# Performance work log

Hardware: AMD Instinct MI355X
Metric: run time of the kernel (lower is better)

Reference implementation:

```python
import jax, jax.numpy as jnp
import numpy as np

N_NODES = 5000
N_EDGES = 40000
NUM_ATOM_TYPES = 100
HID = 32            # multiplicity of 0e and 1o in irreps_hidden
EDGE_ATTR_DIM = 8
NUM_BOND_TYPES = 5
OUT_SCALARS = 2 * 6 + 1  # max_charge=6 -> 13x0e
CUTOFF = 5.0
SQRT3 = 1.7320508075688772


def _sh(edge_vec):
    # o3.SphericalHarmonics('1x0e + 1x1o', normalize=True, normalization='component')
    d = jnp.sqrt(jnp.sum(edge_vec * edge_vec, axis=-1) + 1e-12)
    n = edge_vec / d[:, None]
    sh0 = jnp.ones(edge_vec.shape[0], edge_vec.dtype)          # [E]
    sh1 = SQRT3 * n[:, (1, 2, 0)]                              # [E,3], e3nn (y,z,x) order
    return sh0, sh1, d


def _soft_one_hot(d):
    # e3nn.math.soft_one_hot_linspace(d, 0, cutoff, 8, basis='gaussian', cutoff=True)
    values = jnp.linspace(0.0, CUTOFF, EDGE_ATTR_DIM + 2)[1:-1]
    step = CUTOFF / (EDGE_ATTR_DIM + 1)
    diff = (d[:, None] - values[None, :]) / step
    return jnp.exp(-diff * diff) / 1.12


def _mlp(x, W0, b0, W1, b1):
    # ScalarMLP(in, out, hidden=[in], SiLU)
    return jax.nn.silu(x @ W0 + b0) @ W1 + b1


def _tp_init(s, sh0, sh1, w):
    # FCTP(32x0e, 1x0e+1x1o -> 32x0e+32x1o); paths: 0e*0e->0e, 0e*1o->1o
    E = s.shape[0]
    w1 = w[:, : HID * HID].reshape(E, HID, HID)
    w2 = w[:, HID * HID :].reshape(E, HID, HID)
    c = 1.0 / np.sqrt(HID)  # fan-in = 32 per output irrep
    out_s = c * jnp.einsum('eu,euw->ew', s * sh0[:, None], w1)
    out_v = c * jnp.einsum('eu,ei,euw->ewi', s, sh1, w2)
    return out_s, out_v


def _tp_hidden(s, v, sh0, sh1, w):
    # FCTP(32x0e+32x1o, 1x0e+1x1o -> 32x0e+32x1o)
    # path order: 0e*0e->0e, 0e*1o->1o, 1o*0e->1o, 1o*1o->0e
    E = s.shape[0]
    ws = w.reshape(E, 4, HID, HID)
    c = 1.0 / np.sqrt(2 * HID)  # fan-in = 64 per output irrep
    dot = jnp.einsum('eui,ei->eu', v, sh1) / SQRT3  # CG(1,1->0) = delta/sqrt(3)
    out_s = c * (jnp.einsum('eu,euw->ew', s * sh0[:, None], ws[:, 0]) +
                 jnp.einsum('eu,euw->ew', dot, ws[:, 3]))
    out_v = c * (jnp.einsum('eu,ei,euw->ewi', s, sh1, ws[:, 1]) +
                 jnp.einsum('eui,euw->ewi', v * sh0[:, None, None], ws[:, 2]))
    return out_s, out_v


def _edge_tp(s1, v1, s2, v2, sh0, sh1, w):
    # FCTP(64x0e+64x1o (concat of two hidden), 1x0e+1x1o -> 5x0e)
    # blocks in concat order: s_src, v_src, s_dst, v_dst
    E = s1.shape[0]
    ws = w.reshape(E, 4, HID, NUM_BOND_TYPES)
    c = 1.0 / np.sqrt(4 * HID)  # fan-in = 128
    d1 = jnp.einsum('eui,ei->eu', v1, sh1) / SQRT3
    d2 = jnp.einsum('eui,ei->eu', v2, sh1) / SQRT3
    return c * (jnp.einsum('eu,euw->ew', s1 * sh0[:, None], ws[:, 0]) +
                jnp.einsum('eu,euw->ew', d1, ws[:, 1]) +
                jnp.einsum('eu,euw->ew', s2 * sh0[:, None], ws[:, 2]) +
                jnp.einsum('eu,euw->ew', d2, ws[:, 3]))


def _scatter_mean(ms, mv, dst, n):
    cnt = jax.ops.segment_sum(jnp.ones(dst.shape[0], ms.dtype), dst, num_segments=n)
    cnt = jnp.maximum(cnt, 1.0)
    s = jax.ops.segment_sum(ms, dst, num_segments=n) / cnt[:, None]
    v = jax.ops.segment_sum(mv, dst, num_segments=n) / cnt[:, None, None]
    return s, v


def setup_inputs() -> dict:
    key = jax.random.key(0)
    ks = jax.random.split(key, 16)
    def w(k, shape, fan_in):
        return jax.random.normal(k, shape, dtype=jnp.float32) / np.sqrt(fan_in)
    inp = {}
    inp['coordinates'] = jax.random.normal(ks[0], (N_NODES, 3), dtype=jnp.float32) * 1.5
    inp['atom_types'] = jax.random.randint(ks[1], (N_NODES,), 0, NUM_ATOM_TYPES)
    inp['edge_index'] = jax.random.randint(ks[2], (2, N_EDGES), 0, N_NODES)
    inp['atom_embed'] = jax.random.normal(ks[3], (NUM_ATOM_TYPES, HID), dtype=jnp.float32)
    inp['ip_W0'] = w(ks[4], (EDGE_ATTR_DIM, EDGE_ATTR_DIM), EDGE_ATTR_DIM)
    inp['ip_b0'] = jnp.zeros((EDGE_ATTR_DIM,), jnp.float32)
    inp['ip_W1'] = w(ks[5], (EDGE_ATTR_DIM, 2 * HID * HID), EDGE_ATTR_DIM)
    inp['ip_b1'] = jnp.zeros((2 * HID * HID,), jnp.float32)
    inp['ly_W0'] = w(ks[6], (EDGE_ATTR_DIM, EDGE_ATTR_DIM), EDGE_ATTR_DIM)
    inp['ly_b0'] = jnp.zeros((EDGE_ATTR_DIM,), jnp.float32)
    inp['ly_W1'] = w(ks[7], (EDGE_ATTR_DIM, 4 * HID * HID), EDGE_ATTR_DIM)
    inp['ly_b1'] = jnp.zeros((4 * HID * HID,), jnp.float32)
    inp['ly_Ws'] = jax.random.normal(ks[8], (HID, HID), dtype=jnp.float32)
    inp['ly_Wv'] = jax.random.normal(ks[9], (HID, HID), dtype=jnp.float32)
    inp['et_W0'] = w(ks[10], (EDGE_ATTR_DIM, EDGE_ATTR_DIM), EDGE_ATTR_DIM)
    inp['et_b0'] = jnp.zeros((EDGE_ATTR_DIM,), jnp.float32)
    inp['et_W1'] = w(ks[11], (EDGE_ATTR_DIM, 4 * HID * NUM_BOND_TYPES), EDGE_ATTR_DIM)
    inp['et_b1'] = jnp.zeros((4 * HID * NUM_BOND_TYPES,), jnp.float32)
    inp['no_W1'] = jax.random.normal(ks[12], (HID, OUT_SCALARS), dtype=jnp.float32)
    inp['no_W2'] = jax.random.normal(ks[13], (OUT_SCALARS, OUT_SCALARS), dtype=jnp.float32)
    return inp


def reference(coordinates, atom_types, edge_index, atom_embed,
              ip_W0, ip_b0, ip_W1, ip_b1,
              ly_W0, ly_b0, ly_W1, ly_b1, ly_Ws, ly_Wv,
              et_W0, et_b0, et_W1, et_b1, no_W1, no_W2):
    n = coordinates.shape[0]
    src, dst = edge_index[0], edge_index[1]
    edge_vec = coordinates[dst] - coordinates[src]
    sh0, sh1, d = _sh(edge_vec)
    edge_attr = _soft_one_hot(d)                              # [E,8]
    # initial projector: Conv(32x0e -> 32x0e+32x1o)
    s0 = atom_embed[atom_types]                               # [N,32]
    w_ip = _mlp(edge_attr, ip_W0, ip_b0, ip_W1, ip_b1)        # [E,2048]
    ms, mv = _tp_init(s0[src], sh0, sh1, w_ip)
    s, v = _scatter_mean(ms, mv, dst, n)                      # [N,32],[N,32,3]
    # one LinearSelfInteraction(Conv) layer
    w_ly = _mlp(edge_attr, ly_W0, ly_b0, ly_W1, ly_b1)        # [E,4096]
    ms, mv = _tp_hidden(s[src], v[src], sh0, sh1, w_ly)
    cs, cv = _scatter_mean(ms, mv, dst, n)
    lc = 1.0 / np.sqrt(HID)  # e3nn o3.Linear normalization
    s = cs + lc * (s @ ly_Ws)
    v = cv + lc * jnp.einsum('eui,uw->ewi', v, ly_Wv)
    # edge output: FCTP([h_src, h_dst], edge_sh) with radial weights
    w_et = _mlp(edge_attr, et_W0, et_b0, et_W1, et_b1)        # [E,640]
    edge_out = _edge_tp(s[src], v[src], s[dst], v[dst], sh0, sh1, w_et)  # [E,5]
    # node output MLP on detached scalar channel (13x0e)
    sd = jax.lax.stop_gradient(s)
    h = jax.nn.silu(sd @ no_W1 / np.sqrt(HID))
    node_out = h @ no_W2 / np.sqrt(OUT_SCALARS)               # [N,13]
    return edge_out, node_out
```

## Files before the change

### kernel.cpp

```cpp
#include <hip/hip_runtime.h>

#define NN 5000
#define NE 40000
#define HB 625

typedef unsigned int u32;
typedef unsigned short u16;
typedef __fp16 h16x2 __attribute__((ext_vector_type(2)));
typedef _Float16 f16x8 __attribute__((ext_vector_type(8)));
typedef __attribute__((ext_vector_type(4))) float f32x4;

union AF { u32 u[4]; f16x8 v; uint4 q; };

__device__ __forceinline__ float siluf(float x) { return x / (1.f + __expf(-x)); }

__device__ __forceinline__ u32 f2bf_u(float f) {
  u32 x = __float_as_uint(f);
  return (x + 0x7FFFu + ((x >> 16) & 1u)) >> 16;
}
__device__ __forceinline__ u16 f2bf(float f) { return (u16)f2bf_u(f); }
__device__ __forceinline__ float bf2f(u16 v) { return __uint_as_float(((u32)v) << 16); }
__device__ __forceinline__ u32 packbf2(float lo, float hi) {
  return f2bf_u(lo) | (f2bf_u(hi) << 16);
}
__device__ __forceinline__ u32 pkh2(float a, float b) {
  union { h16x2 h; u32 u; } r;
  r.h = __builtin_amdgcn_cvt_pkrtz(a, b);
  return r.u;
}
__device__ __forceinline__ u16 f2h(float v) {
  _Float16 h = (_Float16)v;
  return *(u16*)&h;
}
__device__ __forceinline__ void unpack8(uint4 q, float* f) {
  f[0] = __uint_as_float(q.x << 16); f[1] = __uint_as_float(q.x & 0xFFFF0000u);
  f[2] = __uint_as_float(q.y << 16); f[3] = __uint_as_float(q.y & 0xFFFF0000u);
  f[4] = __uint_as_float(q.z << 16); f[5] = __uint_as_float(q.z & 0xFFFF0000u);
  f[6] = __uint_as_float(q.w << 16); f[7] = __uint_as_float(q.w & 0xFFFF0000u);
}
__device__ __forceinline__ float dot8f(const float* h, const float* w, float init) {
  float a = init;
#pragma unroll
  for (int k = 0; k < 8; k++) a = fmaf(h[k], w[k], a);
  return a;
}
__device__ __forceinline__ void mlp8(const float* ea, const float* __restrict__ W0,
                                     const float* __restrict__ b0, float* h) {
#pragma unroll
  for (int j = 0; j < 8; j++) {
    float a = b0[j];
#pragma unroll
    for (int i = 0; i < 8; i++) a += ea[i] * W0[i*8 + j];
    h[j] = siluf(a);
  }
}
__device__ __forceinline__ AF mkfrag(float hs, const float* s) {
  AF a;
  a.u[0] = pkh2(hs*s[0], hs*s[1]);
  a.u[1] = pkh2(hs*s[2], hs*s[3]);
  a.u[2] = pkh2(hs*s[4], hs*s[5]);
  a.u[3] = pkh2(hs*s[6], hs*s[7]);
  return a;
}

__global__ __launch_bounds__(256) void k_conv1g(
    const float* __restrict__ coords, const int* __restrict__ eidx,
    const float* __restrict__ emb, const int* __restrict__ atype,
    const float* __restrict__ ipW0, const float* __restrict__ ipb0,
    const float* __restrict__ lyW0, const float* __restrict__ lyb0,
    const float* __restrict__ etW0, const float* __restrict__ etb0,
    const float* __restrict__ W1, const float* __restrict__ b1,
    const float* __restrict__ lyW1, const float* __restrict__ lyb1,
    float* __restrict__ sh, float* __restrict__ h_ly, float* __restrict__ h_et,
    int* __restrict__ cur, int* __restrict__ perm,
    u16* __restrict__ msg, u16* __restrict__ lyT) {
  if (blockIdx.x >= HB) {
    int b = blockIdx.x - HB;
    int h = b >> 3;
    int t0 = (b & 7)*2304 + threadIdx.x*9;
#pragma unroll
    for (int j = 0; j < 9; j++) {
      int t = t0 + j;
      int kch = t >> 9, rem = t & 511;
      int col = rem >> 3, kk = rem & 7;
      int k = kch*8 + kk;
      int basec = (h == 0) ? ((col >> 5)*1024 + (col & 31))
                           : ((col < 32) ? (2048 + col) : (3072 + (col - 32)));
      float v = (k < 256) ? lyW1[(k >> 5)*4096 + basec + (k & 31)*32]
                          : lyb1[basec + (k - 256)*32];
      lyT[h*18432 + t] = f2h(v);
    }
    return;
  }
  __shared__ __align__(16) u16 B2[36*64*8];
  __shared__ float hl[64][9];
  __shared__ float shl[64][4];
  __shared__ int   sAl[64];
  {
    int col = threadIdx.x & 63, pth = col >> 5, w = col & 31;
    int k0 = (threadIdx.x >> 6) * 72;
    for (int k = k0; k < k0 + 72; k++) {
      float v = (k < 256) ? W1[(k >> 5)*2048 + pth*1024 + (k & 31)*32 + w]
                          : b1[pth*1024 + (k - 256)*32 + w];
      B2[((k >> 3)*64 + col)*8 + (k & 7)] = f2h(v);
    }
  }
  if (threadIdx.x < 64) {
    int idx = threadIdx.x;
    int w = (idx >> 4) & 3, m = idx & 15;
    int tile = blockIdx.x*4 + w;
    int e = tile*16 + m;
    int s = eidx[e], d = eidx[NE + e];
    float vx = coords[d*3+0] - coords[s*3+0];
    float vy = coords[d*3+1] - coords[s*3+1];
    float vz = coords[d*3+2] - coords[s*3+2];
    float dist = sqrtf(vx*vx + vy*vy + vz*vz + 1e-12f);
    float inv = 1.f / dist;
    const float SQ3 = 1.7320508075688772f;
    float s0 = SQ3 * vy * inv;
    float s1 = SQ3 * vz * inv;
    float s2 = SQ3 * vx * inv;
    sh[e*3+0] = s0; sh[e*3+1] = s1; sh[e*3+2] = s2;
    shl[idx][0] = s0; shl[idx][1] = s1; shl[idx][2] = s2;
    sAl[idx] = atype[s];
    float ea[8];
    const float step = 5.f / 9.f;
#pragma unroll
    for (int jj = 0; jj < 8; jj++) {
      float diff = (dist - step * (float)(jj+1)) * (9.f / 5.f);
      ea[jj] = __expf(-diff*diff) * (1.f / 1.12f);
    }
    float h[8];
    mlp8(ea, ipW0, ipb0, h);
#pragma unroll
    for (int jj = 0; jj < 8; jj++) hl[idx][jj] = h[jj];
    mlp8(ea, lyW0, lyb0, h);
    { float4 f0 = {h[0],h[1],h[2],h[3]}, f1 = {h[4],h[5],h[6],h[7]};
      *(float4*)&h_ly[e*8] = f0; *(float4*)&h_ly[e*8+4] = f1; }
    mlp8(ea, etW0, etb0, h);
    { float4 f0 = {h[0],h[1],h[2],h[3]}, f1 = {h[4],h[5],h[6],h[7]};
      *(float4*)&h_et[e*8] = f0; *(float4*)&h_et[e*8+4] = f1; }
    int* cp = &cur[d];
    atomicCAS(cp, (int)0xAAAAAAAA, 0);
    int t = atomicAdd(cp, 1);
    if (t < 64) perm[d*64 + t] = e;
  }
  __syncthreads();
  int lane = threadIdx.x & 63;
  int m = lane & 15, q = lane >> 4, wid = threadIdx.x >> 6;
  const float cs = 0.17677669529663687f;
  int tile = blockIdx.x*4 + wid;
  {
    int le = wid*16 + m;
    int srow = sAl[le];
    float4 sA = *(const float4*)&emb[srow*32 + q*8];
    float4 sB = *(const float4*)&emb[srow*32 + q*8 + 4];
    float sf[8] = {sA.x,sA.y,sA.z,sA.w,sB.x,sB.y,sB.z,sB.w};
    float hf[8];
#pragma unroll
    for (int k = 0; k < 8; k++) hf[k] = hl[le][k];
    f32x4 acc0 = {0.f,0.f,0.f,0.f}, acc1 = acc0, acc2 = acc0, acc3 = acc0;
#pragma unroll
    for (int ks = 0; ks < 9; ks++) {
      float hs = (ks < 8) ? hf[ks] : 1.f;
      AF a = mkfrag(hs, sf);
      int c2 = (ks*4 + q)*64;
      AF b0, b1f, b2, b3;
      b0.q  = *(const uint4*)&B2[(c2 +  0 + m)*8];
      b1f.q = *(const uint4*)&B2[(c2 + 16 + m)*8];
      b2.q  = *(const uint4*)&B2[(c2 + 32 + m)*8];
      b3.q  = *(const uint4*)&B2[(c2 + 48 + m)*8];
      acc0 = __builtin_amdgcn_mfma_f32_16x16x32_f16(a.v, b0.v,  acc0, 0, 0, 0);
      acc1 = __builtin_amdgcn_mfma_f32_16x16x32_f16(a.v, b1f.v, acc1, 0, 0, 0);
      acc2 = __builtin_amdgcn_mfma_f32_16x16x32_f16(a.v, b2.v,  acc2, 0, 0, 0);
      acc3 = __builtin_amdgcn_mfma_f32_16x16x32_f16(a.v, b3.v,  acc3, 0, 0, 0);
    }
#pragma unroll
    for (int r = 0; r < 4; r++) {
      int lr = wid*16 + q*4 + r;
      int et = tile*16 + q*4 + r;
      u16* mp = msg + (size_t)et*128;
      mp[m]      = f2bf(cs*acc0[r]);
      mp[16 + m] = f2bf(cs*acc1[r]);
      float s0v = shl[lr][0], s1v = shl[lr][1], s2v = shl[lr][2];
      float m0 = cs*acc2[r], m1 = cs*acc3[r];
      mp[32 +      m] = f2bf(m0*s0v);
      mp[64 +      m] = f2bf(m0*s1v);
      mp[96 +      m] = f2bf(m0*s2v);
      mp[32 + 16 + m] = f2bf(m1*s0v);
      mp[64 + 16 + m] = f2bf(m1*s1v);
      mp[96 + 16 + m] = f2bf(m1*s2v);
    }
  }
}

__global__ __launch_bounds__(256) void k_conv2(
    const float* __restrict__ hE, const float* __restrict__ sh,
    const float* __restrict__ s1, const float* __restrict__ v1soa,
    const int* __restrict__ eidx, const u16* __restrict__ lyT,
    u16* __restrict__ msgA, u16* __restrict__ msgB) {
  __shared__ __align__(16) u16 B2[36*64*8];
  const bool scalarHalf = blockIdx.x < HB;
  int blk = scalarHalf ? blockIdx.x : blockIdx.x - HB;
  {
    const uint4* src4 = (const uint4*)(lyT + (scalarHalf ? 0 : 18432));
    uint4* dst4 = (uint4*)B2;
    for (int t = threadIdx.x; t < 2304; t += 256) dst4[t] = src4[t];
  }
  __syncthreads();
  int lane = threadIdx.x & 63;
  int m = lane & 15, q = lane >> 4, wid = threadIdx.x >> 6;
  const float c = 0.125f;
  int tile = blk*4 + wid;
  {
    int e = tile*16 + m;
    int srcn = eidx[e];
    float4 hA = *(const float4*)&hE[e*8];
    float4 hB = *(const float4*)&hE[e*8 + 4];
    float hf[8] = {hA.x,hA.y,hA.z,hA.w,hB.x,hB.y,hB.z,hB.w};

    if (scalarHalf) {
      float4 sA = *(const float4*)&s1[srcn*32 + q*8];
      float4 sB = *(const float4*)&s1[srcn*32 + q*8 + 4];
      float sf[8] = {sA.x,sA.y,sA.z,sA.w,sB.x,sB.y,sB.z,sB.w};
      f32x4 acc0 = {0.f,0.f,0.f,0.f}, acc1 = acc0, acc2 = acc0, acc3 = acc0;
#pragma unroll
      for (int ks = 0; ks < 9; ks++) {
        float hs = (ks < 8) ? hf[ks] : 1.f;
        AF a = mkfrag(hs, sf);
        int c2 = (ks*4 + q)*64;
        AF b0, b1f, b2, b3;
        b0.q  = *(const uint4*)&B2[(c2 +  0 + m)*8];
        b1f.q = *(const uint4*)&B2[(c2 + 16 + m)*8];
        b2.q  = *(const uint4*)&B2[(c2 + 32 + m)*8];
        b3.q  = *(const uint4*)&B2[(c2 + 48 + m)*8];
        acc0 = __builtin_amdgcn_mfma_f32_16x16x32_f16(a.v, b0.v,  acc0, 0, 0, 0);
        acc1 = __builtin_amdgcn_mfma_f32_16x16x32_f16(a.v, b1f.v, acc1, 0, 0, 0);
        acc2 = __builtin_amdgcn_mfma_f32_16x16x32_f16(a.v, b2.v,  acc2, 0, 0, 0);
        acc3 = __builtin_amdgcn_mfma_f32_16x16x32_f16(a.v, b3.v,  acc3, 0, 0, 0);
      }
#pragma unroll
      for (int r = 0; r < 4; r++) {
        int et = tile*16 + q*4 + r;
        u16* mp = msgA + (size_t)et*128;
        mp[m]      = f2bf(c*acc0[r]);
        mp[16 + m] = f2bf(c*acc1[r]);
        float s0v = sh[et*3+0], s1v = sh[et*3+1], s2v = sh[et*3+2];
        float m0 = c*acc2[r], m1 = c*acc3[r];
        mp[32 +      m] = f2bf(m0*s0v);
        mp[64 +      m] = f2bf(m0*s1v);
        mp[96 +      m] = f2bf(m0*s2v);
        mp[32 + 16 + m] = f2bf(m1*s0v);
        mp[64 + 16 + m] = f2bf(m1*s1v);
        mp[96 + 16 + m] = f2bf(m1*s2v);
      }
    } else {
      const float is3 = 0.5773502691896258f;
      float vf[3][8];
#pragma unroll
      for (int i = 0; i < 3; i++) {
        float4 aa = *(const float4*)&v1soa[i*160000 + srcn*32 + q*8];
        float4 bb = *(const float4*)&v1soa[i*160000 + srcn*32 + q*8 + 4];
        vf[i][0]=aa.x; vf[i][1]=aa.y; vf[i][2]=aa.z; vf[i][3]=aa.w;
        vf[i][4]=bb.x; vf[i][5]=bb.y; vf[i][6]=bb.z; vf[i][7]=bb.w;
      }
      float es0 = sh[e*3+0], es1 = sh[e*3+1], es2 = sh[e*3+2];
      float df[8];
#pragma unroll
      for (int j = 0; j < 8; j++)
        df[j] = (vf[0][j]*es0 + vf[1][j]*es1 + vf[2][j]*es2) * is3;
      f32x4 z = {0.f,0.f,0.f,0.f};
      f32x4 aV00 = z, aV01 = z, aV10 = z, aV11 = z, aV20 = z, aV21 = z, aD0 = z, aD1 = z;
#pragma unroll
      for (int ks = 0; ks < 9; ks++) {
        float hs = (ks < 8) ? hf[ks] : 1.f;
        int c2 = (ks*4 + q)*64;
        AF b0, b1f, b2, b3;
        b0.q  = *(const uint4*)&B2[(c2 +  0 + m)*8];
        b1f.q = *(const uint4*)&B2[(c2 + 16 + m)*8];
        b2.q  = *(const uint4*)&B2[(c2 + 32 + m)*8];
        b3.q  = *(const uint4*)&B2[(c2 + 48 + m)*8];
        AF a0 = mkfrag(hs, vf[0]);
        AF a1 = mkfrag(hs, vf[1]);
        AF a2 = mkfrag(hs, vf[2]);
        AF ad = mkfrag(hs, df);
        aV00 = __builtin_amdgcn_mfma_f32_16x16x32_f16(a0.v, b0.v,  aV00, 0, 0, 0);
        aV01 = __builtin_amdgcn_mfma_f32_16x16x32_f16(a0.v, b1f.v, aV01, 0, 0, 0);
        aV10 = __builtin_amdgcn_mfma_f32_16x16x32_f16(a1.v, b0.v,  aV10, 0, 0, 0);
        aV11 = __builtin_amdgcn_mfma_f32_16x16x32_f16(a1.v, b1f.v, aV11, 0, 0, 0);
        aV20 = __builtin_amdgcn_mfma_f32_16x16x32_f16(a2.v, b0.v,  aV20, 0, 0, 0);
        aV21 = __builtin_amdgcn_mfma_f32_16x16x32_f16(a2.v, b1f.v, aV21, 0, 0, 0);
        aD0  = __builtin_amdgcn_mfma_f32_16x16x32_f16(ad.v, b2.v,  aD0,  0, 0, 0);
        aD1  = __builtin_amdgcn_mfma_f32_16x16x32_f16(ad.v, b3.v,  aD1,  0, 0, 0);
      }
#pragma unroll
      for (int r = 0; r < 4; r++) {
        int et = tile*16 + q*4 + r;
        u16* mp = msgB + (size_t)et*128;
        mp[m]      = f2bf(c*aD0[r]);
        mp[16 + m] = f2bf(c*aD1[r]);
        mp[32 +      m] = f2bf(c*aV00[r]);
        mp[32 + 16 + m] = f2bf(c*aV01[r]);
        mp[64 +      m] = f2bf(c*aV10[r]);
        mp[64 + 16 + m] = f2bf(c*aV11[r]);
        mp[96 +      m] = f2bf(c*aV20[r]);
        mp[96 + 16 + m] = f2bf(c*aV21[r]);
      }
    }
  }
}

__global__ __launch_bounds__(256) void k_gather1(
    const u16* __restrict__ msg, const int* __restrict__ perm,
    const int* __restrict__ cur, float* __restrict__ s1,
    float* __restrict__ v1soa) {
  __shared__ int pe[2][64];
  int ln = threadIdx.x >> 7, c = threadIdx.x & 127;
  int n = blockIdx.x*2 + ln;
  int deg = min(cur[n], 64);
  if (c < 64) pe[ln][c] = perm[n*64 + c];
  __syncthreads();
  float acc = 0.f;
  int j = 0;
  for (; j + 4 <= deg; j += 4) {
    int e0 = pe[ln][j], e1 = pe[ln][j+1], e2 = pe[ln][j+2], e3 = pe[ln][j+3];
    float x0 = bf2f(msg[(size_t)e0*128 + c]);
    float x1 = bf2f(msg[(size_t)e1*128 + c]);
    float x2 = bf2f(msg[(size_t)e2*128 + c]);
    float x3 = bf2f(msg[(size_t)e3*128 + c]);
    acc += (x0 + x1) + (x2 + x3);
  }
  for (; j < deg; j++)
    acc += bf2f(msg[(size_t)pe[ln][j]*128 + c]);
  acc /= (float)max(deg, 1);
  if (c < 32) s1[n*32 + c] = acc;
  else { int i = (c-32) >> 5, w = (c-32) & 31; v1soa[i*160000 + n*32 + w] = acc; }
}

__global__ __launch_bounds__(256) void k_gather2(
    const u16* __restrict__ msgA, const u16* __restrict__ msgB,
    const int* __restrict__ perm, const int* __restrict__ cur,
    const float* __restrict__ s1, const float* __restrict__ v1soa,
    const float* __restrict__ Ws, const float* __restrict__ Wv,
    const float* __restrict__ noW1, const float* __restrict__ noW2,
    float* __restrict__ s2, float* __restrict__ v2, float* __restrict__ outN) {
  __shared__ int pe[2][64];
  __shared__ float sb[2][32];
  __shared__ float hb[2][13];
  int ln = threadIdx.x >> 7, c = threadIdx.x & 127;
  int n = blockIdx.x*2 + ln;
  int deg = min(cur[n], 64);
  if (c < 64) pe[ln][c] = perm[n*64 + c];
  __syncthreads();
  float acc = 0.f;
  int j = 0;
  for (; j + 4 <= deg; j += 4) {
    int e0 = pe[ln][j], e1 = pe[ln][j+1], e2 = pe[ln][j+2], e3 = pe[ln][j+3];
    float x0 = bf2f(msgA[(size_t)e0*128 + c]) + bf2f(msgB[(size_t)e0*128 + c]);
    float x1 = bf2f(msgA[(size_t)e1*128 + c]) + bf2f(msgB[(size_t)e1*128 + c]);
    float x2 = bf2f(msgA[(size_t)e2*128 + c]) + bf2f(msgB[(size_t)e2*128 + c]);
    float x3 = bf2f(msgA[(size_t)e3*128 + c]) + bf2f(msgB[(size_t)e3*128 + c]);
    acc += (x0 + x1) + (x2 + x3);
  }
  for (; j < deg; j++) {
    int e = pe[ln][j];
    acc += bf2f(msgA[(size_t)e*128 + c]) + bf2f(msgB[(size_t)e*128 + c]);
  }
  acc /= (float)max(deg, 1);
  const float lc = 0.17677669529663687f;
  if (c < 32) {
    float ss = 0.f;
#pragma unroll 8
    for (int u = 0; u < 32; u++) ss += s1[n*32 + u] * Ws[u*32 + c];
    float val = acc + lc*ss;
    s2[n*32 + c] = val;
    sb[ln][c] = val;
  } else {
    int i = (c-32) >> 5, w = (c-32) & 31;
    float sv = 0.f;
#pragma unroll 8
    for (int u = 0; u < 32; u++) sv += v1soa[i*160000 + n*32 + u] * Wv[u*32 + w];
    v2[n*96 + w*3 + i] = acc + lc*sv;
  }
  __syncthreads();
  const float i32 = 0.17677669529663687f;
  if (c < 13) {
    float a = 0.f;
#pragma unroll 8
    for (int u = 0; u < 32; u++) a += sb[ln][u] * noW1[u*13 + c];
    hb[ln][c] = siluf(a * i32);
  }
  __syncthreads();
  const float i13 = 0.2773500981126146f;
  if (c < 13) {
    float a = 0.f;
#pragma unroll
    for (int j2 = 0; j2 < 13; j2++) a += hb[ln][j2] * noW2[j2*13 + c];
    outN[n*13 + c] = a * i13;
  }
}

__global__ __launch_bounds__(256) void k_e3(
    const float* __restrict__ hE, const float* __restrict__ sh,
    const float* __restrict__ s2, const float* __restrict__ v2,
    const int* __restrict__ eidx,
    const float* __restrict__ W1, const float* __restrict__ b1,
    float* __restrict__ out) {
  __shared__ uint4 WQ[640];
  __shared__ float BQ[640];
  for (int t = threadIdx.x; t < 640; t += 256) {
    int u = t & 31, pw = t >> 5, p2 = pw / 5, w = pw - p2*5;
    int col = p2*160 + u*5 + w;
    const float* s = W1 + col;
    uint4 q;
    q.x = packbf2(s[0],      s[640]);
    q.y = packbf2(s[1280],   s[1920]);
    q.z = packbf2(s[2560],   s[3200]);
    q.w = packbf2(s[3840],   s[4480]);
    WQ[t] = q;
    BQ[t] = b1[col];
  }
  __syncthreads();
  const int g = threadIdx.x >> 5, tw = threadIdx.x & 31;
  const float c = 0.08838834764831845f;
  const float is3 = 0.5773502691896258f;
  for (int p = blockIdx.x*8 + g; p*2 < NE; p += gridDim.x*8) {
    int e0 = p*2, e1 = e0 + 1;
    float h0[8], h1[8];
    {
      float4 qa = *(const float4*)&hE[e0*8];
      float4 qb = *(const float4*)&hE[e0*8+4];
      h0[0]=qa.x; h0[1]=qa.y; h0[2]=qa.z; h0[3]=qa.w;
      h0[4]=qb.x; h0[5]=qb.y; h0[6]=qb.z; h0[7]=qb.w;
      float4 qc = *(const float4*)&hE[e1*8];
      float4 qd = *(const float4*)&hE[e1*8+4];
      h1[0]=qc.x; h1[1]=qc.y; h1[2]=qc.z; h1[3]=qc.w;
      h1[4]=qd.x; h1[5]=qd.y; h1[6]=qd.z; h1[7]=qd.w;
    }
    int sA = eidx[e0], dA = eidx[NE+e0];
    int sB = eidx[e1], dB = eidx[NE+e1];
    float sa0 = sh[e0*3+0], sa1 = sh[e0*3+1], sa2 = sh[e0*3+2];
    float sb0 = sh[e1*3+0], sb1 = sh[e1*3+1], sb2 = sh[e1*3+2];
    float c00 = s2[sA*32 + tw];
    float c01 = (v2[sA*96+tw*3+0]*sa0 + v2[sA*96+tw*3+1]*sa1 + v2[sA*96+tw*3+2]*sa2) * is3;
    float c02 = s2[dA*32 + tw];
    float c03 = (v2[dA*96+tw*3+0]*sa0 + v2[dA*96+tw*3+1]*sa1 + v2[dA*96+tw*3+2]*sa2) * is3;
    float c10 = s2[sB*32 + tw];
    float c11 = (v2[sB*96+tw*3+0]*sb0 + v2[sB*96+tw*3+1]*sb1 + v2[sB*96+tw*3+2]*sb2) * is3;
    float c12 = s2[dB*32 + tw];
    float c13 = (v2[dB*96+tw*3+0]*sb0 + v2[dB*96+tw*3+1]*sb1 + v2[dB*96+tw*3+2]*sb2) * is3;
    float part0[5] = {0,0,0,0,0};
    float part1[5] = {0,0,0,0,0};
#pragma unroll
    for (int pp = 0; pp < 4; pp++) {
      float cp0 = (pp==0) ? c00 : (pp==1) ? c01 : (pp==2) ? c02 : c03;
      float cp1 = (pp==0) ? c10 : (pp==1) ? c11 : (pp==2) ? c12 : c13;
#pragma unroll
      for (int w = 0; w < 5; w++) {
        int idx = (pp*5 + w)*32 + tw;
        float f[8];
        unpack8(WQ[idx], f);
        float bv = BQ[idx];
        part0[w] = fmaf(cp0, dot8f(h0, f, bv), part0[w]);
        part1[w] = fmaf(cp1, dot8f(h1, f, bv), part1[w]);
      }
    }
#pragma unroll
    for (int off = 16; off > 0; off >>= 1)
#pragma unroll
      for (int w = 0; w < 5; w++) {
        part0[w] += __shfl_xor(part0[w], off, 32);
        part1[w] += __shfl_xor(part1[w], off, 32);
      }
    float outv = 0.f;
#pragma unroll
    for (int w = 0; w < 5; w++) {
      if (tw == w)     outv = part0[w];
      if (tw == 5 + w) outv = part1[w];
    }
    if (tw < 10) out[e0*5 + tw] = c * outv;
  }
}

extern "C" void kernel_launch(void* const* d_in, const int* in_sizes, int n_in,
                              void* d_out, int out_size, void* d_ws, size_t ws_size,
                              hipStream_t stream) {
  (void)in_sizes; (void)n_in; (void)out_size; (void)ws_size;
  const float* coords = (const float*)d_in[0];
  const int*   atype  = (const int*)d_in[1];
  const int*   eidx   = (const int*)d_in[2];
  const float* emb    = (const float*)d_in[3];
  const float* ipW0 = (const float*)d_in[4];
  const float* ipb0 = (const float*)d_in[5];
  const float* ipW1 = (const float*)d_in[6];
  const float* ipb1 = (const float*)d_in[7];
  const float* lyW0 = (const float*)d_in[8];
  const float* lyb0 = (const float*)d_in[9];
  const float* lyW1 = (const float*)d_in[10];
  const float* lyb1 = (const float*)d_in[11];
  const float* lyWs = (const float*)d_in[12];
  const float* lyWv = (const float*)d_in[13];
  const float* etW0 = (const float*)d_in[14];
  const float* etb0 = (const float*)d_in[15];
  const float* etW1 = (const float*)d_in[16];
  const float* etb1 = (const float*)d_in[17];
  const float* noW1 = (const float*)d_in[18];
  const float* noW2 = (const float*)d_in[19];

  float* ws = (float*)d_ws;
  float* sh    = ws;
  float* h_ly  = ws + 440000;
  float* h_et  = ws + 760000;
  float* s1    = ws + 1240000;
  float* v1soa = ws + 1400000;
  float* s2    = ws + 1880000;
  float* v2    = ws + 2040000;
  int*   cur   = (int*)(ws + 2520000);
  int*   perm  = (int*)(ws + 2525000);
  u16*   msgA  = (u16*)(ws + 2845000);
  u16*   msgB  = (u16*)(ws + 5405000);
  u16*   lyT   = (u16*)(ws + 7965000);

  float* outE = (float*)d_out;
  float* outN = (float*)d_out + NE*5;

  k_conv1g<<<HB + 16, 256, 0, stream>>>(coords, eidx, emb, atype,
                                        ipW0, ipb0, lyW0, lyb0, etW0, etb0,
                                        ipW1, ipb1, lyW1, lyb1,
                                        sh, h_ly, h_et, cur, perm, msgA, lyT);
  k_gather1<<<NN/2, 256, 0, stream>>>(msgA, perm, cur, s1, v1soa);
  k_conv2<<<2*HB, 256, 0, stream>>>(h_ly, sh, s1, v1soa, eidx, lyT, msgA, msgB);
  k_gather2<<<NN/2, 256, 0, stream>>>(msgA, msgB, perm, cur, s1, v1soa,
                                      lyWs, lyWv, noW1, noW2, s2, v2, outN);
  k_e3<<<2500, 256, 0, stream>>>(h_et, sh, s2, v2, eidx, etW1, etb1, outE);
}
```

Before: 177.9 us.

## Read transposed weights from global memory instead of staging in LDS, add prep kernel

Adds a separate prep kernel that converts the initial-projector and layer weights to fp16 MFMA layout, so the conv kernels read B fragments directly from global/L2 instead of filling shared memory per block. k_conv1 now has every lane compute edge geometry and the radial MLP redundantly, and uses shuffles instead of LDS and barriers. The k_e3 grid drops from 2500 to 1024 blocks. It trades LDS fill and sync cost for redundant ALU work, repeated global weight reads and one extra launch.

Result: faster. 164.9 us (-7.3%).

```diff
diff --git a/kernel.cpp b/kernel.cpp
--- a/kernel.cpp
+++ b/kernel.cpp
@@ -2,7 +2,6 @@
 
 #define NN 5000
 #define NE 40000
-#define HB 625
 
 typedef unsigned int u32;
 typedef unsigned short u16;
@@ -19,7 +18,6 @@
   return (x + 0x7FFFu + ((x >> 16) & 1u)) >> 16;
 }
 __device__ __forceinline__ u16 f2bf(float f) { return (u16)f2bf_u(f); }
-__device__ __forceinline__ float bf2f(u16 v) { return __uint_as_float(((u32)v) << 16); }
 __device__ __forceinline__ u32 packbf2(float lo, float hi) {
   return f2bf_u(lo) | (f2bf_u(hi) << 16);
 }
@@ -63,19 +61,12 @@
   return a;
 }
 
-__global__ __launch_bounds__(256) void k_conv1g(
-    const float* __restrict__ coords, const int* __restrict__ eidx,
-    const float* __restrict__ emb, const int* __restrict__ atype,
-    const float* __restrict__ ipW0, const float* __restrict__ ipb0,
-    const float* __restrict__ lyW0, const float* __restrict__ lyb0,
-    const float* __restrict__ etW0, const float* __restrict__ etb0,
-    const float* __restrict__ W1, const float* __restrict__ b1,
+__global__ __launch_bounds__(256) void k_prep(
+    const float* __restrict__ ipW1, const float* __restrict__ ipb1,
     const float* __restrict__ lyW1, const float* __restrict__ lyb1,
-    float* __restrict__ sh, float* __restrict__ h_ly, float* __restrict__ h_et,
-    int* __restrict__ cur, int* __restrict__ perm,
-    u16* __restrict__ msg, u16* __restrict__ lyT) {
-  if (blockIdx.x >= HB) {
-    int b = blockIdx.x - HB;
+    u16* __restrict__ ipT, u16* __restrict__ lyT) {
+  int b = blockIdx.x;
+  if (b < 16) {
     int h = b >> 3;
     int t0 = (b & 7)*2304 + threadIdx.x*9;
 #pragma unroll
@@ -90,75 +81,129 @@
                           : lyb1[basec + (k - 256)*32];
       lyT[h*18432 + t] = f2h(v);
     }
-    return;
-  }
-  __shared__ __align__(16) u16 B2[36*64*8];
-  __shared__ float hl[64][9];
-  __shared__ float shl[64][4];
-  __shared__ int   sAl[64];
-  {
-    int col = threadIdx.x & 63, pth = col >> 5, w = col & 31;
-    int k0 = (threadIdx.x >> 6) * 72;
-    for (int k = k0; k < k0 + 72; k++) {
-      float v = (k < 256) ? W1[(k >> 5)*2048 + pth*1024 + (k & 31)*32 + w]
-                          : b1[pth*1024 + (k - 256)*32 + w];
-      B2[((k >> 3)*64 + col)*8 + (k & 7)] = f2h(v);
-    }
-  }
-  if (threadIdx.x < 64) {
-    int idx = threadIdx.x;
-    int w = (idx >> 4) & 3, m = idx & 15;
-    int tile = blockIdx.x*4 + w;
-    int e = tile*16 + m;
-    int s = eidx[e], d = eidx[NE + e];
-    float vx = coords[d*3+0] - coords[s*3+0];
-    float vy = coords[d*3+1] - coords[s*3+1];
-    float vz = coords[d*3+2] - coords[s*3+2];
-    float dist = sqrtf(vx*vx + vy*vy + vz*vz + 1e-12f);
-    float inv = 1.f / dist;
-    const float SQ3 = 1.7320508075688772f;
-    float s0 = SQ3 * vy * inv;
-    float s1 = SQ3 * vz * inv;
-    float s2 = SQ3 * vx * inv;
-    sh[e*3+0] = s0; sh[e*3+1] = s1; sh[e*3+2] = s2;
-    shl[idx][0] = s0; shl[idx][1] = s1; shl[idx][2] = s2;
-    sAl[idx] = atype[s];
-    float ea[8];
-    const float step = 5.f / 9.f;
-#pragma unroll
-    for (int jj = 0; jj < 8; jj++) {
-      float diff = (dist - step * (float)(jj+1)) * (9.f / 5.f);
-      ea[jj] = __expf(-diff*diff) * (1.f / 1.12f);
-    }
-    float h[8];
-    mlp8(ea, ipW0, ipb0, h);
-#pragma unroll
-    for (int jj = 0; jj < 8; jj++) hl[idx][jj] = h[jj];
-    mlp8(ea, lyW0, lyb0, h);
-    { float4 f0 = {h[0],h[1],h[2],h[3]}, f1 = {h[4],h[5],h[6],h[7]};
+  } else {
+    int t0 = (b - 16)*2304 + threadIdx.x*9;
+#pragma unroll
+    for (int j = 0; j < 9; j++) {
+      int t = t0 + j;
+      int kch = t >> 9, rem = t & 511;
+      int col = rem >> 3, kk = rem & 7;
+      int k = kch*8 + kk;
+      int pth = col >> 5, w = col & 31;
+      float v = (k < 256) ? ipW1[(k >> 5)*2048 + pth*1024 + (k & 31)*32 + w]
+                          : ipb1[pth*1024 + (k - 256)*32 + w];
+      ipT[t] = f2h(v);
+    }
+  }
+}
+
+__global__ __launch_bounds__(256) void k_conv1(
+    const float* __restrict__ coords, const int* __restrict__ eidx,
+    const float* __restrict__ emb, const int* __restrict__ atype,
+    const float* __restrict__ ipW0, const float* __restrict__ ipb0,
+    const float* __restrict__ lyW0, const float* __restrict__ lyb0,
+    const float* __restrict__ etW0, const float* __restrict__ etb0,
+    const u16* __restrict__ ipT,
+    float* __restrict__ sh, float* __restrict__ h_ly, float* __restrict__ h_et,
+    int* __restrict__ cur, int* __restrict__ perm, u16* __restrict__ msg) {
+  int wid = threadIdx.x >> 6, lane = threadIdx.x & 63;
+  int tile = blockIdx.x*4 + wid;
+  int m = lane & 15, q = lane >> 4;
+  int e = tile*16 + m;
+  int s = eidx[e], d = eidx[NE + e];
+  float vx = coords[d*3+0] - coords[s*3+0];
+  float vy = coords[d*3+1] - coords[s*3+1];
+  float vz = coords[d*3+2] - coords[s*3+2];
+  float dist = sqrtf(vx*vx + vy*vy + vz*vz + 1e-12f);
+  float dinv = 1.f / dist;
+  const float SQ3 = 1.7320508075688772f;
+  float sh0 = SQ3 * vy * dinv;
+  float sh1 = SQ3 * vz * dinv;
+  float sh2 = SQ3 * vx * dinv;
+  int srow = atype[s];
+  float ea[8];
+  const float step = 5.f / 9.f;
+#pragma unroll
+  for (int jj = 0; jj < 8; jj++) {
+    float diff = (dist - step * (float)(jj+1)) * (9.f / 5.f);
+    ea[jj] = __expf(-diff*diff) * (1.f / 1.12f);
+  }
+  float hip[8], hly[8], het[8];
+  mlp8(ea, ipW0, ipb0, hip);
+  mlp8(ea, lyW0, lyb0, hly);
+  mlp8(ea, etW0, etb0, het);
+  if (q == 0) {
+    sh[e*3+0] = sh0; sh[e*3+1] = sh1; sh[e*3+2] = sh2;
+    { float4 f0 = {hly[0],hly[1],hly[2],hly[3]}, f1 = {hly[4],hly[5],hly[6],hly[7]};
       *(float4*)&h_ly[e*8] = f0; *(float4*)&h_ly[e*8+4] = f1; }
-    mlp8(ea, etW0, etb0, h);
-    { float4 f0 = {h[0],h[1],h[2],h[3]}, f1 = {h[4],h[5],h[6],h[7]};
+    { float4 f0 = {het[0],het[1],het[2],het[3]}, f1 = {het[4],het[5],het[6],het[7]};
       *(float4*)&h_et[e*8] = f0; *(float4*)&h_et[e*8+4] = f1; }
     int* cp = &cur[d];
     atomicCAS(cp, (int)0xAAAAAAAA, 0);
     int t = atomicAdd(cp, 1);
     if (t < 64) perm[d*64 + t] = e;
   }
-  __syncthreads();
-  int lane = threadIdx.x & 63;
-  int m = lane & 15, q = lane >> 4, wid = threadIdx.x >> 6;
+  float4 sA = *(const float4*)&emb[srow*32 + q*8];
+  float4 sB = *(const float4*)&emb[srow*32 + q*8 + 4];
+  float sf[8] = {sA.x,sA.y,sA.z,sA.w,sB.x,sB.y,sB.z,sB.w};
+  f32x4 acc0 = {0.f,0.f,0.f,0.f}, acc1 = acc0, acc2 = acc0, acc3 = acc0;
   const float cs = 0.17677669529663687f;
-  int tile = blockIdx.x*4 + wid;
-  {
-    int le = wid*16 + m;
-    int srow = sAl[le];
-    float4 sA = *(const float4*)&emb[srow*32 + q*8];
-    float4 sB = *(const float4*)&emb[srow*32 + q*8 + 4];
+#pragma unroll
+  for (int ks = 0; ks < 9; ks++) {
+    float hs = (ks < 8) ? hip[ks] : 1.f;
+    AF a = mkfrag(hs, sf);
+    int c2 = (ks*4 + q)*64;
+    AF b0, b1f, b2, b3;
+    b0.q  = *(const uint4*)&ipT[(c2 +  0 + m)*8];
+    b1f.q = *(const uint4*)&ipT[(c2 + 16 + m)*8];
+    b2.q  = *(const uint4*)&ipT[(c2 + 32 + m)*8];
+    b3.q  = *(const uint4*)&ipT[(c2 + 48 + m)*8];
+    acc0 = __builtin_amdgcn_mfma_f32_16x16x32_f16(a.v, b0.v,  acc0, 0, 0, 0);
+    acc1 = __builtin_amdgcn_mfma_f32_16x16x32_f16(a.v, b1f.v, acc1, 0, 0, 0);
+    acc2 = __builtin_amdgcn_mfma_f32_16x16x32_f16(a.v, b2.v,  acc2, 0, 0, 0);
+    acc3 = __builtin_amdgcn_mfma_f32_16x16x32_f16(a.v, b3.v,  acc3, 0, 0, 0);
+  }
+#pragma unroll
+  for (int r = 0; r < 4; r++) {
+    int et = tile*16 + q*4 + r;
+    u16* mp = msg + (size_t)et*128;
+    mp[m]      = f2bf(cs*acc0[r]);
+    mp[16 + m] = f2bf(cs*acc1[r]);
+    float s0v = __shfl(sh0, q*4 + r, 64);
+    float s1v = __shfl(sh1, q*4 + r, 64);
+    float s2v = __shfl(sh2, q*4 + r, 64);
+    float m0 = cs*acc2[r], m1 = cs*acc3[r];
+    mp[32 +      m] = f2bf(m0*s0v);
+    mp[64 +      m] = f2bf(m0*s1v);
+    mp[96 +      m] = f2bf(m0*s2v);
+    mp[32 + 16 + m] = f2bf(m1*s0v);
+    mp[64 + 16 + m] = f2bf(m1*s1v);
+    mp[96 + 16 + m] = f2bf(m1*s2v);
+  }
+}
+
+__global__ __launch_bounds__(256) void k_conv2(
+    const float* __restrict__ hE, const float* __restrict__ sh,
+    const float* __restrict__ s1, const float* __restrict__ v1soa,
+    const int* __restrict__ eidx, const u16* __restrict__ lyT,
+    u16* __restrict__ msgA, u16* __restrict__ msgB) {
+  int wid = threadIdx.x >> 6, lane = threadIdx.x & 63;
+  const bool scalarHalf = blockIdx.x < 625;
+  int blk = scalarHalf ? blockIdx.x : blockIdx.x - 625;
+  int tile = blk*4 + wid;
+  int m = lane & 15, q = lane >> 4;
+  const u16* Bg = lyT + (scalarHalf ? 0 : 18432);
+  const float c = 0.125f;
+  int e = tile*16 + m;
+  int srcn = eidx[e];
+  float4 hA = *(const float4*)&hE[e*8];
+  float4 hB = *(const float4*)&hE[e*8 + 4];
+  float hf[8] = {hA.x,hA.y,hA.z,hA.w,hB.x,hB.y,hB.z,hB.w};
+
+  if (scalarHalf) {
+    float4 sA = *(const float4*)&s1[srcn*32 + q*8];
+    float4 sB = *(const float4*)&s1[srcn*32 + q*8 + 4];
     float sf[8] = {sA.x,sA.y,sA.z,sA.w,sB.x,sB.y,sB.z,sB.w};
-    float hf[8];
-#pragma unroll
-    for (int k = 0; k < 8; k++) hf[k] = hl[le][k];
     f32x4 acc0 = {0.f,0.f,0.f,0.f}, acc1 = acc0, acc2 = acc0, acc3 = acc0;
 #pragma unroll
     for (int ks = 0; ks < 9; ks++) {
@@ -166,10 +211,10 @@
       AF a = mkfrag(hs, sf);
       int c2 = (ks*4 + q)*64;
       AF b0, b1f, b2, b3;
-      b0.q  = *(const uint4*)&B2[(c2 +  0 + m)*8];
-      b1f.q = *(const uint4*)&B2[(c2 + 16 + m)*8];
-      b2.q  = *(const uint4*)&B2[(c2 + 32 + m)*8];
-      b3.q  = *(const uint4*)&B2[(c2 + 48 + m)*8];
+      b0.q  = *(const uint4*)&Bg[(c2 +  0 + m)*8];
+      b1f.q = *(const uint4*)&Bg[(c2 + 16 + m)*8];
+      b2.q  = *(const uint4*)&Bg[(c2 + 32 + m)*8];
+      b3.q  = *(const uint4*)&Bg[(c2 + 48 + m)*8];
       acc0 = __builtin_amdgcn_mfma_f32_16x16x32_f16(a.v, b0.v,  acc0, 0, 0, 0);
       acc1 = __builtin_amdgcn_mfma_f32_16x16x32_f16(a.v, b1f.v, acc1, 0, 0, 0);
       acc2 = __builtin_amdgcn_mfma_f32_16x16x32_f16(a.v, b2.v,  acc2, 0, 0, 0);
@@ -177,13 +222,12 @@
     }
 #pragma unroll
     for (int r = 0; r < 4; r++) {
-      int lr = wid*16 + q*4 + r;
       int et = tile*16 + q*4 + r;
-      u16* mp = msg + (size_t)et*128;
-      mp[m]      = f2bf(cs*acc0[r]);
-      mp[16 + m] = f2bf(cs*acc1[r]);
-      float s0v = shl[lr][0], s1v = shl[lr][1], s2v = shl[lr][2];
-      float m0 = cs*acc2[r], m1 = cs*acc3[r];
+      u16* mp = msgA + (size_t)et*128;
+      mp[m]      = f2bf(c*acc0[r]);
+      mp[16 + m] = f2bf(c*acc1[r]);
+      float s0v = sh[et*3+0], s1v = sh[et*3+1], s2v = sh[et*3+2];
+      float m0 = c*acc2[r], m1 = c*acc3[r];
       mp[32 +      m] = f2bf(m0*s0v);
       mp[64 +      m] = f2bf(m0*s1v);
       mp[96 +      m] = f2bf(m0*s2v);
@@ -191,121 +235,57 @@
       mp[64 + 16 + m] = f2bf(m1*s1v);
       mp[96 + 16 + m] = f2bf(m1*s2v);
     }
-  }
-}
-
-__global__ __launch_bounds__(256) void k_conv2(
-    const float* __restrict__ hE, const float* __restrict__ sh,
-    const float* __restrict__ s1, const float* __restrict__ v1soa,
-    const int* __restrict__ eidx, const u16* __restrict__ lyT,
-    u16* __restrict__ msgA, u16* __restrict__ msgB) {
-  __shared__ __align__(16) u16 B2[36*64*8];
-  const bool scalarHalf = blockIdx.x < HB;
-  int blk = scalarHalf ? blockIdx.x : blockIdx.x - HB;
-  {
-    const uint4* src4 = (const uint4*)(lyT + (scalarHalf ? 0 : 18432));
-    uint4* dst4 = (uint4*)B2;
-    for (int t = threadIdx.x; t < 2304; t += 256) dst4[t] = src4[t];
-  }
-  __syncthreads();
-  int lane = threadIdx.x & 63;
-  int m = lane & 15, q = lane >> 4, wid = threadIdx.x >> 6;
-  const float c = 0.125f;
-  int tile = blk*4 + wid;
-  {
-    int e = tile*16 + m;
-    int srcn = eidx[e];
-    float4 hA = *(const float4*)&hE[e*8];
-    float4 hB = *(const float4*)&hE[e*8 + 4];
-    float hf[8] = {hA.x,hA.y,hA.z,hA.w,hB.x,hB.y,hB.z,hB.w};
-
-    if (scalarHalf) {
-      float4 sA = *(const float4*)&s1[srcn*32 + q*8];
-      float4 sB = *(const float4*)&s1[srcn*32 + q*8 + 4];
-      float sf[8] = {sA.x,sA.y,sA.z,sA.w,sB.x,sB.y,sB.z,sB.w};
-      f32x4 acc0 = {0.f,0.f,0.f,0.f}, acc1 = acc0, acc2 = acc0, acc3 = acc0;
-#pragma unroll
-      for (int ks = 0; ks < 9; ks++) {
-        float hs = (ks < 8) ? hf[ks] : 1.f;
-        AF a = mkfrag(hs, sf);
-        int c2 = (ks*4 + q)*64;
-        AF b0, b1f, b2, b3;
-        b0.q  = *(const uint4*)&B2[(c2 +  0 + m)*8];
-        b1f.q = *(const uint4*)&B2[(c2 + 16 + m)*8];
-        b2.q  = *(const uint4*)&B2[(c2 + 32 + m)*8];
-        b3.q  = *(const uint4*)&B2[(c2 + 48 + m)*8];
-        acc0 = __builtin_amdgcn_mfma_f32_16x16x32_f16(a.v, b0.v,  acc0, 0, 0, 0);
-        acc1 = __builtin_amdgcn_mfma_f32_16x16x32_f16(a.v, b1f.v, acc1, 0, 0, 0);
-        acc2 = __builtin_amdgcn_mfma_f32_16x16x32_f16(a.v, b2.v,  acc2, 0, 0, 0);
-        acc3 = __builtin_amdgcn_mfma_f32_16x16x32_f16(a.v, b3.v,  acc3, 0, 0, 0);
-      }
-#pragma unroll
-      for (int r = 0; r < 4; r++) {
-        int et = tile*16 + q*4 + r;
-        u16* mp = msgA + (size_t)et*128;
-        mp[m]      = f2bf(c*acc0[r]);
-        mp[16 + m] = f2bf(c*acc1[r]);
-        float s0v = sh[et*3+0], s1v = sh[et*3+1], s2v = sh[et*3+2];
-        float m0 = c*acc2[r], m1 = c*acc3[r];
-        mp[32 +      m] = f2bf(m0*s0v);
-        mp[64 +      m] = f2bf(m0*s1v);
-        mp[96 +      m] = f2bf(m0*s2v);
-        mp[32 + 16 + m] = f2bf(m1*s0v);
-        mp[64 + 16 + m] = f2bf(m1*s1v);
-        mp[96 + 16 + m] = f2bf(m1*s2v);
-      }
-    } else {
-      const float is3 = 0.5773502691896258f;
-      float vf[3][8];
-#pragma unroll
-      for (int i = 0; i < 3; i++) {
-        float4 aa = *(const float4*)&v1soa[i*160000 + srcn*32 + q*8];
-        float4 bb = *(const float4*)&v1soa[i*160000 + srcn*32 + q*8 + 4];
-        vf[i][0]=aa.x; vf[i][1]=aa.y; vf[i][2]=aa.z; vf[i][3]=aa.w;
-        vf[i][4]=bb.x; vf[i][5]=bb.y; vf[i][6]=bb.z; vf[i][7]=bb.w;
-      }
-      float es0 = sh[e*3+0], es1 = sh[e*3+1], es2 = sh[e*3+2];
-      float df[8];
-#pragma unroll
-      for (int j = 0; j < 8; j++)
-        df[j] = (vf[0][j]*es0 + vf[1][j]*es1 + vf[2][j]*es2) * is3;
-      f32x4 z = {0.f,0.f,0.f,0.f};
-      f32x4 aV00 = z, aV01 = z, aV10 = z, aV11 = z, aV20 = z, aV21 = z, aD0 = z, aD1 = z;
-#pragma unroll
-      for (int ks = 0; ks < 9; ks++) {
-        float hs = (ks < 8) ? hf[ks] : 1.f;
-        int c2 = (ks*4 + q)*64;
-        AF b0, b1f, b2, b3;
-        b0.q  = *(const uint4*)&B2[(c2 +  0 + m)*8];
-        b1f.q = *(const uint4*)&B2[(c2 + 16 + m)*8];
-        b2.q  = *(const uint4*)&B2[(c2 + 32 + m)*8];
-        b3.q  = *(const uint4*)&B2[(c2 + 48 + m)*8];
-        AF a0 = mkfrag(hs, vf[0]);
-        AF a1 = mkfrag(hs, vf[1]);
-        AF a2 = mkfrag(hs, vf[2]);
-        AF ad = mkfrag(hs, df);
-        aV00 = __builtin_amdgcn_mfma_f32_16x16x32_f16(a0.v, b0.v,  aV00, 0, 0, 0);
-        aV01 = __builtin_amdgcn_mfma_f32_16x16x32_f16(a0.v, b1f.v, aV01, 0, 0, 0);
-        aV10 = __builtin_amdgcn_mfma_f32_16x16x32_f16(a1.v, b0.v,  aV10, 0, 0, 0);
-        aV11 = __builtin_amdgcn_mfma_f32_16x16x32_f16(a1.v, b1f.v, aV11, 0, 0, 0);
-        aV20 = __builtin_amdgcn_mfma_f32_16x16x32_f16(a2.v, b0.v,  aV20, 0, 0, 0);
-        aV21 = __builtin_amdgcn_mfma_f32_16x16x32_f16(a2.v, b1f.v, aV21, 0, 0, 0);
-        aD0  = __builtin_amdgcn_mfma_f32_16x16x32_f16(ad.v, b2.v,  aD0,  0, 0, 0);
-        aD1  = __builtin_amdgcn_mfma_f32_16x16x32_f16(ad.v, b3.v,  aD1,  0, 0, 0);
-      }
-#pragma unroll
-      for (int r = 0; r < 4; r++) {
-        int et = tile*16 + q*4 + r;
-        u16* mp = msgB + (size_t)et*128;
-        mp[m]      = f2bf(c*aD0[r]);
-        mp[16 + m] = f2bf(c*aD1[r]);
-        mp[32 +      m] = f2bf(c*aV00[r]);
-        mp[32 + 16 + m] = f2bf(c*aV01[r]);
-        mp[64 +      m] = f2bf(c*aV10[r]);
-        mp[64 + 16 + m] = f2bf(c*aV11[r]);
-        mp[96 +      m] = f2bf(c*aV20[r]);
-        mp[96 + 16 + m] = f2bf(c*aV21[r]);
-      }
+  } else {
+    const float is3 = 0.5773502691896258f;
+    float vf[3][8];
+#pragma unroll
+    for (int i = 0; i < 3; i++) {
+      float4 aa = *(const float4*)&v1soa[i*160000 + srcn*32 + q*8];
+      float4 bb = *(const float4*)&v1soa[i*160000 + srcn*32 + q*8 + 4];
+      vf[i][0]=aa.x; vf[i][1]=aa.y; vf[i][2]=aa.z; vf[i][3]=aa.w;
+      vf[i][4]=bb.x; vf[i][5]=bb.y; vf[i][6]=bb.z; vf[i][7]=bb.w;
+    }
+    float es0 = sh[e*3+0], es1 = sh[e*3+1], es2 = sh[e*3+2];
+    float df[8];
+#pragma unroll
+    for (int j = 0; j < 8; j++)
+      df[j] = (vf[0][j]*es0 + vf[1][j]*es1 + vf[2][j]*es2) * is3;
+    f32x4 z = {0.f,0.f,0.f,0.f};
+    f32x4 aV00 = z, aV01 = z, aV10 = z, aV11 = z, aV20 = z, aV21 = z, aD0 = z, aD1 = z;
+#pragma unroll
+    for (int ks = 0; ks < 9; ks++) {
+      float hs = (ks < 8) ? hf[ks] : 1.f;
+      int c2 = (ks*4 + q)*64;
+      AF b0, b1f, b2, b3;
+      b0.q  = *(const uint4*)&Bg[(c2 +  0 + m)*8];
+      b1f.q = *(const uint4*)&Bg[(c2 + 16 + m)*8];
+      b2.q  = *(const uint4*)&Bg[(c2 + 32 + m)*8];
+      b3.q  = *(const uint4*)&Bg[(c2 + 48 + m)*8];
+      AF a0 = mkfrag(hs, vf[0]);
+      AF a1 = mkfrag(hs, vf[1]);
+      AF a2 = mkfrag(hs, vf[2]);
+      AF ad = mkfrag(hs, df);
+      aV00 = __builtin_amdgcn_mfma_f32_16x16x32_f16(a0.v, b0.v,  aV00, 0, 0, 0);
+      aV01 = __builtin_amdgcn_mfma_f32_16x16x32_f16(a0.v, b1f.v, aV01, 0, 0, 0);
+      aV10 = __builtin_amdgcn_mfma_f32_16x16x32_f16(a1.v, b0.v,  aV10, 0, 0, 0);
+      aV11 = __builtin_amdgcn_mfma_f32_16x16x32_f16(a1.v, b1f.v, aV11, 0, 0, 0);
+      aV20 = __builtin_amdgcn_mfma_f32_16x16x32_f16(a2.v, b0.v,  aV20, 0, 0, 0);
+      aV21 = __builtin_amdgcn_mfma_f32_16x16x32_f16(a2.v, b1f.v, aV21, 0, 0, 0);
+      aD0  = __builtin_amdgcn_mfma_f32_16x16x32_f16(ad.v, b2.v,  aD0,  0, 0, 0);
+      aD1  = __builtin_amdgcn_mfma_f32_16x16x32_f16(ad.v, b3.v,  aD1,  0, 0, 0);
+    }
+#pragma unroll
+    for (int r = 0; r < 4; r++) {
+      int et = tile*16 + q*4 + r;
+      u16* mp = msgB + (size_t)et*128;
+      mp[m]      = f2bf(c*aD0[r]);
+      mp[16 + m] = f2bf(c*aD1[r]);
+      mp[32 +      m] = f2bf(c*aV00[r]);
+      mp[32 + 16 + m] = f2bf(c*aV01[r]);
+      mp[64 +      m] = f2bf(c*aV10[r]);
+      mp[64 + 16 + m] = f2bf(c*aV11[r]);
+      mp[96 +      m] = f2bf(c*aV20[r]);
+      mp[96 + 16 + m] = f2bf(c*aV21[r]);
     }
   }
 }
@@ -324,14 +304,14 @@
   int j = 0;
   for (; j + 4 <= deg; j += 4) {
     int e0 = pe[ln][j], e1 = pe[ln][j+1], e2 = pe[ln][j+2], e3 = pe[ln][j+3];
-    float x0 = bf2f(msg[(size_t)e0*128 + c]);
-    float x1 = bf2f(msg[(size_t)e1*128 + c]);
-    float x2 = bf2f(msg[(size_t)e2*128 + c]);
-    float x3 = bf2f(msg[(size_t)e3*128 + c]);
+    float x0 = __uint_as_float(((u32)msg[(size_t)e0*128 + c]) << 16);
+    float x1 = __uint_as_float(((u32)msg[(size_t)e1*128 + c]) << 16);
+    float x2 = __uint_as_float(((u32)msg[(size_t)e2*128 + c]) << 16);
+    float x3 = __uint_as_float(((u32)msg[(size_t)e3*128 + c]) << 16);
     acc += (x0 + x1) + (x2 + x3);
   }
   for (; j < deg; j++)
-    acc += bf2f(msg[(size_t)pe[ln][j]*128 + c]);
+    acc += __uint_as_float(((u32)msg[(size_t)pe[ln][j]*128 + c]) << 16);
   acc /= (float)max(deg, 1);
   if (c < 32) s1[n*32 + c] = acc;
   else { int i = (c-32) >> 5, w = (c-32) & 31; v1soa[i*160000 + n*32 + w] = acc; }
@@ -356,15 +336,20 @@
   int j = 0;
   for (; j + 4 <= deg; j += 4) {
     int e0 = pe[ln][j], e1 = pe[ln][j+1], e2 = pe[ln][j+2], e3 = pe[ln][j+3];
-    float x0 = bf2f(msgA[(size_t)e0*128 + c]) + bf2f(msgB[(size_t)e0*128 + c]);
-    float x1 = bf2f(msgA[(size_t)e1*128 + c]) + bf2f(msgB[(size_t)e1*128 + c]);
-    float x2 = bf2f(msgA[(size_t)e2*128 + c]) + bf2f(msgB[(size_t)e2*128 + c]);
-    float x3 = bf2f(msgA[(size_t)e3*128 + c]) + bf2f(msgB[(size_t)e3*128 + c]);
+    float x0 = __uint_as_float(((u32)msgA[(size_t)e0*128 + c]) << 16)
+             + __uint_as_float(((u32)msgB[(size_t)e0*128 + c]) << 16);
+    float x1 = __uint_as_float(((u32)msgA[(size_t)e1*128 + c]) << 16)
+             + __uint_as_float(((u32)msgB[(size_t)e1*128 + c]) << 16);
+    float x2 = __uint_as_float(((u32)msgA[(size_t)e2*128 + c]) << 16)
+             + __uint_as_float(((u32)msgB[(size_t)e2*128 + c]) << 16);
+    float x3 = __uint_as_float(((u32)msgA[(size_t)e3*128 + c]) << 16)
+             + __uint_as_float(((u32)msgB[(size_t)e3*128 + c]) << 16);
     acc += (x0 + x1) + (x2 + x3);
   }
   for (; j < deg; j++) {
     int e = pe[ln][j];
-    acc += bf2f(msgA[(size_t)e*128 + c]) + bf2f(msgB[(size_t)e*128 + c]);
+    acc += __uint_as_float(((u32)msgA[(size_t)e*128 + c]) << 16)
+         + __uint_as_float(((u32)msgB[(size_t)e*128 + c]) << 16);
   }
   acc /= (float)max(deg, 1);
   const float lc = 0.17677669529663687f;
@@ -520,17 +505,18 @@
   u16*   msgA  = (u16*)(ws + 2845000);
   u16*   msgB  = (u16*)(ws + 5405000);
   u16*   lyT   = (u16*)(ws + 7965000);
+  u16*   ipT   = (u16*)(ws + 7983432);
 
   float* outE = (float*)d_out;
   float* outN = (float*)d_out + NE*5;
 
-  k_conv1g<<<HB + 16, 256, 0, stream>>>(coords, eidx, emb, atype,
-                                        ipW0, ipb0, lyW0, lyb0, etW0, etb0,
-                                        ipW1, ipb1, lyW1, lyb1,
-                                        sh, h_ly, h_et, cur, perm, msgA, lyT);
+  k_prep<<<24, 256, 0, stream>>>(ipW1, ipb1, lyW1, lyb1, ipT, lyT);
+  k_conv1<<<625, 256, 0, stream>>>(coords, eidx, emb, atype,
+                                   ipW0, ipb0, lyW0, lyb0, etW0, etb0,
+                                   ipT, sh, h_ly, h_et, cur, perm, msgA);
   k_gather1<<<NN/2, 256, 0, stream>>>(msgA, perm, cur, s1, v1soa);
-  k_conv2<<<2*HB, 256, 0, stream>>>(h_ly, sh, s1, v1soa, eidx, lyT, msgA, msgB);
+  k_conv2<<<1250, 256, 0, stream>>>(h_ly, sh, s1, v1soa, eidx, lyT, msgA, msgB);
   k_gather2<<<NN/2, 256, 0, stream>>>(msgA, msgB, perm, cur, s1, v1soa,
                                       lyWs, lyWv, noW1, noW2, s2, v2, outN);
-  k_e3<<<2500, 256, 0, stream>>>(h_et, sh, s2, v2, eidx, etW1, etb1, outE);
-}
+  k_e3<<<1024, 256, 0, stream>>>(h_et, sh, s2, v2, eidx, etW1, etb1, outE);
+}
```
